# Kernel tuning notes

Measured on AMD Instinct MI355X. Metric: run time of the kernel, lower is better.

## Reference

```python
import jax, jax.numpy as jnp
import numpy as np

OUTPUT_DIM = 2000
INPUT_DIM = 8192
N_COLS = 2000  # must equal OUTPUT_DIM so bias broadcasts over last dim as in the torch code
SPARSITY = 0.9
BLOCK = 4


def _apply_block_sparsity(weight, block=BLOCK, sparsity=SPARSITY, seed=1234):
    # Zero out 4x4 blocks with probability `sparsity`, mirroring apply_block_sparsity.
    rng = np.random.RandomState(seed)
    rb = (weight.shape[0] + block - 1) // block
    cb = (weight.shape[1] + block - 1) // block
    keep = (rng.rand(rb, cb) <= (1.0 - sparsity)).astype(np.float32)
    mask = np.kron(keep, np.ones((block, block), dtype=np.float32))
    return weight * mask[: weight.shape[0], : weight.shape[1]]


def setup_inputs() -> dict:
    key = jax.random.key(0)
    k_w, k_b, k_x = jax.random.split(key, 3)
    weight = np.asarray(jax.random.normal(k_w, (OUTPUT_DIM, INPUT_DIM), dtype=jnp.float32))
    weight = jnp.asarray(_apply_block_sparsity(weight))
    bias = jax.random.normal(k_b, (OUTPUT_DIM,), dtype=jnp.float32)
    x = jax.random.normal(k_x, (INPUT_DIM, N_COLS), dtype=jnp.float32)
    return {"weight": weight, "bias": bias, "x": x}


def reference(weight, bias, x):
    # [OUT, IN] @ [IN, N] -> [OUT, N]; bias [OUT] broadcasts over last dim (N == OUT here),
    # exactly matching torch.matmul(weight, x) + bias.
    return jnp.matmul(weight, x) + bias
```

## Files before the change

kernel.cpp:

```cpp
#include <hip/hip_runtime.h>

#define K_DIM 8192
#define M_REAL 2000
#define N_REAL 2000
#define M_PAD 2048
#define N_PAD 2048

#define BM 128
#define BN 128
#define BK 32

typedef __bf16 bf16x8 __attribute__((ext_vector_type(8)));
typedef float f32x4 __attribute__((ext_vector_type(4)));

__device__ __forceinline__ unsigned short f2bf(float f) {
    union { float f; unsigned u; } v; v.f = f;
    unsigned r = v.u + 0x7FFFu + ((v.u >> 16) & 1u);
    return (unsigned short)(r >> 16);
}

__device__ __forceinline__ void async16(const void* g, void* l) {
    __builtin_amdgcn_global_load_lds((__attribute__((address_space(1))) void*)(g),
                                     (__attribute__((address_space(3))) void*)(l),
                                     16, 0, 0);
}

__global__ __launch_bounds__(256) void conv_w_kernel(const float* __restrict__ W,
                                                     unsigned short* __restrict__ Wb) {
    long long t = (long long)blockIdx.x * 256 + threadIdx.x;
    long long e = t * 8;
    int m = (int)(e >> 13);
    ushort4 o0 = make_ushort4(0, 0, 0, 0), o1 = o0;
    if (m < M_REAL) {
        const float4* src = (const float4*)(W + e);
        float4 f0 = src[0], f1 = src[1];
        o0.x = f2bf(f0.x); o0.y = f2bf(f0.y); o0.z = f2bf(f0.z); o0.w = f2bf(f0.w);
        o1.x = f2bf(f1.x); o1.y = f2bf(f1.y); o1.z = f2bf(f1.z); o1.w = f2bf(f1.w);
    }
    *(ushort4*)(Wb + e) = o0;
    *(ushort4*)(Wb + e + 4) = o1;
}

__global__ __launch_bounds__(256) void conv_xt_kernel(const float* __restrict__ X,
                                                      unsigned short* __restrict__ XT) {
    __shared__ unsigned short tile[64][65];
    int k0 = blockIdx.x * 64;
    int n0 = blockIdx.y * 64;
    int tx = threadIdx.x & 63;
    int ty = threadIdx.x >> 6;
    int n = n0 + tx;
#pragma unroll
    for (int it = 0; it < 16; ++it) {
        int k = k0 + ty + it * 4;
        float v = (n < N_REAL) ? X[(long long)k * N_REAL + n] : 0.0f;
        tile[ty + it * 4][tx] = f2bf(v);
    }
    __syncthreads();
    int kx = (threadIdx.x & 31) * 2;
    int ny = threadIdx.x >> 5;
#pragma unroll
    for (int it = 0; it < 8; ++it) {
        int nn = ny + it * 8;
        unsigned a = tile[kx][nn];
        unsigned b = tile[kx + 1][nn];
        *(unsigned*)(&XT[(long long)(n0 + nn) * K_DIM + k0 + kx]) = a | (b << 16);
    }
}

__global__ __launch_bounds__(256) void gemm_kernel(const unsigned short* __restrict__ Wb,
                                                   const unsigned short* __restrict__ XT,
                                                   const float* __restrict__ bias,
                                                   float* __restrict__ out) {
    __shared__ __align__(16) unsigned short As[BM * BK];
    __shared__ __align__(16) unsigned short Bs[BN * BK];

    int t = threadIdx.x;
    int w = t >> 6;
    int l = t & 63;
    int wm = (w >> 1) * 64;
    int wn = (w & 1) * 64;
    int lane16 = l & 15;
    int quad = l >> 4;
    int m0 = blockIdx.y * BM;
    int n0 = blockIdx.x * BN;

    f32x4 acc[4][4] = {};

    int srow = l >> 2;
    int scol = (l & 3) * 8;
    int rb = w * 32;
    const unsigned short* gA0 = Wb + (long long)(m0 + rb + srow) * K_DIM + scol;
    const unsigned short* gA1 = gA0 + 16LL * K_DIM;
    const unsigned short* gB0 = XT + (long long)(n0 + rb + srow) * K_DIM + scol;
    const unsigned short* gB1 = gB0 + 16LL * K_DIM;
    unsigned short* lA0 = &As[rb * BK];
    unsigned short* lA1 = &As[(rb + 16) * BK];
    unsigned short* lB0 = &Bs[rb * BK];
    unsigned short* lB1 = &Bs[(rb + 16) * BK];

    for (int kt = 0; kt < K_DIM / BK; ++kt) {
        async16(gA0, lA0);
        async16(gA1, lA1);
        async16(gB0, lB0);
        async16(gB1, lB1);
        gA0 += BK; gA1 += BK; gB0 += BK; gB1 += BK;
        __builtin_amdgcn_s_waitcnt(0);
        __syncthreads();

        bf16x8 a[4], b[4];
#pragma unroll
        for (int i = 0; i < 4; ++i)
            a[i] = *(const bf16x8*)&As[(wm + i * 16 + lane16) * BK + quad * 8];
#pragma unroll
        for (int j = 0; j < 4; ++j)
            b[j] = *(const bf16x8*)&Bs[(wn + j * 16 + lane16) * BK + quad * 8];

#pragma unroll
        for (int i = 0; i < 4; ++i)
#pragma unroll
            for (int j = 0; j < 4; ++j)
                acc[i][j] = __builtin_amdgcn_mfma_f32_16x16x32_bf16(a[i], b[j], acc[i][j], 0, 0, 0);

        __syncthreads();
    }

#pragma unroll
    for (int j = 0; j < 4; ++j) {
        int n = n0 + wn + j * 16 + lane16;
        if (n >= N_REAL) continue;
        float bv = bias[n];
#pragma unroll
        for (int i = 0; i < 4; ++i) {
            int mbase = m0 + wm + i * 16 + quad * 4;
#pragma unroll
            for (int r = 0; r < 4; ++r) {
                int m = mbase + r;
                if (m < M_REAL)
                    out[(long long)m * N_REAL + n] = acc[i][j][r] + bv;
            }
        }
    }
}

extern "C" void kernel_launch(void* const* d_in, const int* in_sizes, int n_in,
                              void* d_out, int out_size, void* d_ws, size_t ws_size,
                              hipStream_t stream) {
    const float* W    = (const float*)d_in[0];
    const float* bias = (const float*)d_in[1];
    const float* X    = (const float*)d_in[2];
    float* out = (float*)d_out;

    unsigned short* Wb = (unsigned short*)d_ws;
    unsigned short* XT = Wb + (long long)M_PAD * K_DIM;

    conv_w_kernel<<<(M_PAD * K_DIM) / (8 * 256), 256, 0, stream>>>(W, Wb);

    dim3 tgrid(K_DIM / 64, N_PAD / 64);
    conv_xt_kernel<<<tgrid, 256, 0, stream>>>(X, XT);

    dim3 ggrid(N_PAD / BN, M_PAD / BM);
    gemm_kernel<<<ggrid, 256, 0, stream>>>(Wb, XT, bias, out);
}
```

Measured before the change: 306.0 us.

## Split GEMM K dimension four ways with atomic accumulation and fuse prep kernels

The GEMM grid gains a K-split dimension of 4, so each block reduces a quarter of K and adds its partial result into the output with atomicAdd. This raises the block count from 256 to 1024, giving the GPU more concurrent work to hide the unpipelined load latency. The weight conversion, the X transpose-conversion and a new bias-initialisation of the output are merged into one prep launch. The cost is four times the output write traffic as atomics, plus a dependency on the output being pre-initialised with bias.

After: 288.8 us. 1.06x faster.

```diff
diff --git a/kernel.cpp b/kernel.cpp
--- a/kernel.cpp
+++ b/kernel.cpp
@@ -9,6 +9,12 @@
 #define BM 128
 #define BN 128
 #define BK 32
+#define SPLITK 4
+#define KSLAB (K_DIM / SPLITK)
+
+#define NB_CONVW 8192
+#define NB_CONVX 4096
+#define NB_INIT  3907
 
 typedef __bf16 bf16x8 __attribute__((ext_vector_type(8)));
 typedef float f32x4 __attribute__((ext_vector_type(4)));
@@ -25,51 +31,63 @@
                                      16, 0, 0);
 }
 
-__global__ __launch_bounds__(256) void conv_w_kernel(const float* __restrict__ W,
-                                                     unsigned short* __restrict__ Wb) {
-    long long t = (long long)blockIdx.x * 256 + threadIdx.x;
-    long long e = t * 8;
-    int m = (int)(e >> 13);
-    ushort4 o0 = make_ushort4(0, 0, 0, 0), o1 = o0;
-    if (m < M_REAL) {
-        const float4* src = (const float4*)(W + e);
-        float4 f0 = src[0], f1 = src[1];
-        o0.x = f2bf(f0.x); o0.y = f2bf(f0.y); o0.z = f2bf(f0.z); o0.w = f2bf(f0.w);
-        o1.x = f2bf(f1.x); o1.y = f2bf(f1.y); o1.z = f2bf(f1.z); o1.w = f2bf(f1.w);
-    }
-    *(ushort4*)(Wb + e) = o0;
-    *(ushort4*)(Wb + e + 4) = o1;
-}
-
-__global__ __launch_bounds__(256) void conv_xt_kernel(const float* __restrict__ X,
-                                                      unsigned short* __restrict__ XT) {
+__global__ __launch_bounds__(256) void prep_kernel(const float* __restrict__ W,
+                                                   const float* __restrict__ X,
+                                                   const float* __restrict__ bias,
+                                                   unsigned short* __restrict__ Wb,
+                                                   unsigned short* __restrict__ XT,
+                                                   float* __restrict__ out) {
     __shared__ unsigned short tile[64][65];
-    int k0 = blockIdx.x * 64;
-    int n0 = blockIdx.y * 64;
-    int tx = threadIdx.x & 63;
-    int ty = threadIdx.x >> 6;
-    int n = n0 + tx;
+    int bid = blockIdx.x;
+    if (bid < NB_CONVW) {
+        long long t = (long long)bid * 256 + threadIdx.x;
+        long long e = t * 8;
+        int m = (int)(e >> 13);
+        ushort4 o0 = make_ushort4(0, 0, 0, 0), o1 = o0;
+        if (m < M_REAL) {
+            const float4* src = (const float4*)(W + e);
+            float4 f0 = src[0], f1 = src[1];
+            o0.x = f2bf(f0.x); o0.y = f2bf(f0.y); o0.z = f2bf(f0.z); o0.w = f2bf(f0.w);
+            o1.x = f2bf(f1.x); o1.y = f2bf(f1.y); o1.z = f2bf(f1.z); o1.w = f2bf(f1.w);
+        }
+        *(ushort4*)(Wb + e) = o0;
+        *(ushort4*)(Wb + e + 4) = o1;
+    } else if (bid < NB_CONVW + NB_CONVX) {
+        int b2 = bid - NB_CONVW;
+        int k0 = (b2 & 127) * 64;
+        int n0 = (b2 >> 7) * 64;
+        int tx = threadIdx.x & 63;
+        int ty = threadIdx.x >> 6;
+        int n = n0 + tx;
 #pragma unroll
-    for (int it = 0; it < 16; ++it) {
-        int k = k0 + ty + it * 4;
-        float v = (n < N_REAL) ? X[(long long)k * N_REAL + n] : 0.0f;
-        tile[ty + it * 4][tx] = f2bf(v);
-    }
-    __syncthreads();
-    int kx = (threadIdx.x & 31) * 2;
-    int ny = threadIdx.x >> 5;
+        for (int it = 0; it < 16; ++it) {
+            int k = k0 + ty + it * 4;
+            float v = (n < N_REAL) ? X[(long long)k * N_REAL + n] : 0.0f;
+            tile[ty + it * 4][tx] = f2bf(v);
+        }
+        __syncthreads();
+        int kx = (threadIdx.x & 31) * 2;
+        int ny = threadIdx.x >> 5;
 #pragma unroll
-    for (int it = 0; it < 8; ++it) {
-        int nn = ny + it * 8;
-        unsigned a = tile[kx][nn];
-        unsigned b = tile[kx + 1][nn];
-        *(unsigned*)(&XT[(long long)(n0 + nn) * K_DIM + k0 + kx]) = a | (b << 16);
+        for (int it = 0; it < 8; ++it) {
+            int nn = ny + it * 8;
+            unsigned a = tile[kx][nn];
+            unsigned b = tile[kx + 1][nn];
+            *(unsigned*)(&XT[(long long)(n0 + nn) * K_DIM + k0 + kx]) = a | (b << 16);
+        }
+    } else {
+        int t = (bid - NB_CONVW - NB_CONVX) * 256 + threadIdx.x;
+        if (t < M_REAL * (N_REAL / 4)) {
+            int m = t / (N_REAL / 4);
+            int n4 = t - m * (N_REAL / 4);
+            float4 bv = *(const float4*)(bias + n4 * 4);
+            *(float4*)(out + (long long)m * N_REAL + n4 * 4) = bv;
+        }
     }
 }
 
 __global__ __launch_bounds__(256) void gemm_kernel(const unsigned short* __restrict__ Wb,
                                                    const unsigned short* __restrict__ XT,
-                                                   const float* __restrict__ bias,
                                                    float* __restrict__ out) {
     __shared__ __align__(16) unsigned short As[BM * BK];
     __shared__ __align__(16) unsigned short Bs[BN * BK];
@@ -83,22 +101,23 @@
     int quad = l >> 4;
     int m0 = blockIdx.y * BM;
     int n0 = blockIdx.x * BN;
+    int ks = blockIdx.z * KSLAB;
 
     f32x4 acc[4][4] = {};
 
     int srow = l >> 2;
     int scol = (l & 3) * 8;
     int rb = w * 32;
-    const unsigned short* gA0 = Wb + (long long)(m0 + rb + srow) * K_DIM + scol;
+    const unsigned short* gA0 = Wb + (long long)(m0 + rb + srow) * K_DIM + ks + scol;
     const unsigned short* gA1 = gA0 + 16LL * K_DIM;
-    const unsigned short* gB0 = XT + (long long)(n0 + rb + srow) * K_DIM + scol;
+    const unsigned short* gB0 = XT + (long long)(n0 + rb + srow) * K_DIM + ks + scol;
     const unsigned short* gB1 = gB0 + 16LL * K_DIM;
     unsigned short* lA0 = &As[rb * BK];
     unsigned short* lA1 = &As[(rb + 16) * BK];
     unsigned short* lB0 = &Bs[rb * BK];
     unsigned short* lB1 = &Bs[(rb + 16) * BK];
 
-    for (int kt = 0; kt < K_DIM / BK; ++kt) {
+    for (int kt = 0; kt < KSLAB / BK; ++kt) {
         async16(gA0, lA0);
         async16(gA1, lA1);
         async16(gB0, lB0);
@@ -128,7 +147,6 @@
     for (int j = 0; j < 4; ++j) {
         int n = n0 + wn + j * 16 + lane16;
         if (n >= N_REAL) continue;
-        float bv = bias[n];
 #pragma unroll
         for (int i = 0; i < 4; ++i) {
             int mbase = m0 + wm + i * 16 + quad * 4;
@@ -136,7 +154,7 @@
             for (int r = 0; r < 4; ++r) {
                 int m = mbase + r;
                 if (m < M_REAL)
-                    out[(long long)m * N_REAL + n] = acc[i][j][r] + bv;
+                    atomicAdd(&out[(long long)m * N_REAL + n], acc[i][j][r]);
             }
         }
     }
@@ -153,11 +171,8 @@
     unsigned short* Wb = (unsigned short*)d_ws;
     unsigned short* XT = Wb + (long long)M_PAD * K_DIM;
 
-    conv_w_kernel<<<(M_PAD * K_DIM) / (8 * 256), 256, 0, stream>>>(W, Wb);
+    prep_kernel<<<NB_CONVW + NB_CONVX + NB_INIT, 256, 0, stream>>>(W, X, bias, Wb, XT, out);
 
-    dim3 tgrid(K_DIM / 64, N_PAD / 64);
-    conv_xt_kernel<<<tgrid, 256, 0, stream>>>(X, XT);
-
-    dim3 ggrid(N_PAD / BN, M_PAD / BM);
-    gemm_kernel<<<ggrid, 256, 0, stream>>>(Wb, XT, bias, out);
+    dim3 ggrid(N_PAD / BN, M_PAD / BM, SPLITK);
+    gemm_kernel<<<ggrid, 256, 0, stream>>>(Wb, XT, out);
 }
```
